# Kernel optimization log

Measured on AMD Instinct MI355X. Metric: run time of the kernel, lower is better.

Reference implementation:

```python
import jax, jax.numpy as jnp
import numpy as np


def setup_inputs() -> dict:
    key = jax.random.key(0)
    kx, ky = jax.random.split(key)
    B, N, M, D = 8, 4096, 4096, 128
    x = jax.random.normal(kx, (B, N, D), dtype=jnp.float32)
    y = jax.random.normal(ky, (B, M, D), dtype=jnp.float32)
    return {"x": x, "y": y}


def reference(x, y):
    # Pairwise L2 distances, equivalent to torch.cdist(x, y) (p=2).
    # ||x_i - y_j||^2 = ||x_i||^2 + ||y_j||^2 - 2 <x_i, y_j>
    x2 = jnp.sum(x * x, axis=-1)[:, :, None]          # [B, N, 1]
    y2 = jnp.sum(y * y, axis=-1)[:, None, :]          # [B, 1, M]
    xy = jnp.einsum("bnd,bmd->bnm", x, y)             # [B, N, M]
    D = jnp.sqrt(jnp.maximum(x2 + y2 - 2.0 * xy, 0.0))  # [B, N, M]
    coverage = D.min(axis=1).mean(axis=-1)            # min over N -> [B, M] -> [B]
    precision = D.min(axis=2).mean(axis=-1)           # min over M -> [B, N] -> [B]
    return (coverage + precision).mean()              # scalar Chamfer loss
```

## Files before the change

kernel.cpp:

```cpp
#include <hip/hip_runtime.h>
#include <cstdint>


#define B_   8
#define N_   4096
#define M_   4096
#define D_   128
#define TPB  8
#define ROWS_PB 256
#define XG   (N_ / ROWS_PB)
#define CHUNKS (M_ / (TPB * 64))

typedef __bf16 bf16x8 __attribute__((ext_vector_type(8)));
typedef float  f32x4  __attribute__((ext_vector_type(4)));
typedef unsigned int u32;

static __device__ __forceinline__ unsigned short f2bf(float f) {
  unsigned u = __float_as_uint(f);
  u += 0x7FFFu + ((u >> 16) & 1u);
  return (unsigned short)(u >> 16);
}

static __device__ __forceinline__ void gld16(void* lds, const void* g) {
  __builtin_amdgcn_global_load_lds(
      (const __attribute__((address_space(1))) void*)g,
      (__attribute__((address_space(3))) void*)lds, 16, 0, 0);
}

__global__ __launch_bounds__(256) void pass1_prep(
    const float* __restrict__ x, const float* __restrict__ y,
    unsigned short* __restrict__ xb, unsigned short* __restrict__ yb,
    float* __restrict__ x2, float* __restrict__ y2)
{
  const int ROWS = B_ * N_;
  int gw   = (blockIdx.x * 256 + threadIdx.x) >> 6;
  int lane = threadIdx.x & 63;
  int half = lane >> 5, sub = lane & 31;
  int row2 = gw * 2 + half;
  bool isx = row2 < ROWS;
  const float* src; unsigned short* dst; float* nrm; int row;
  if (isx) { src = x; dst = xb; nrm = x2; row = row2; }
  else     { src = y; dst = yb; nrm = y2; row = row2 - ROWS; }
  size_t base = (size_t)row * D_ + sub * 4;
  float4 v = *(const float4*)(src + base);
  float sx = isx ? -2.0f : 1.0f;
  u32 p0 = (u32)f2bf(sx * v.x) | ((u32)f2bf(sx * v.y) << 16);
  u32 p1 = (u32)f2bf(sx * v.z) | ((u32)f2bf(sx * v.w) << 16);
  *(uint2*)(dst + base) = make_uint2(p0, p1);
  float s = v.x * v.x + v.y * v.y + v.z * v.z + v.w * v.w;
  #pragma unroll
  for (int m = 1; m < 32; m <<= 1) s += __shfl_xor(s, m, 64);
  if (sub == 0) nrm[row] = s;
}

__global__ __launch_bounds__(256) void pass2_tile(
    const unsigned short* __restrict__ xb, const unsigned short* __restrict__ yb,
    const float* __restrict__ x2, const float* __restrict__ y2,
    float* __restrict__ rowpart, float* __restrict__ colpart)
{
  __shared__ unsigned short ys[2 * 8192];
  __shared__ float cminW[2][16 * 64];

  const int tid  = threadIdx.x;
  const int wave = tid >> 6;
  const int lane = tid & 63;
  const int quad = lane >> 4;
  const int l15  = lane & 15;

  const int id    = blockIdx.x;
  const int b     = id & 7;
  const int xg    = (id >> 3) & 15;
  const int chunk = id >> 7;
  const int n0    = xg * ROWS_PB;
  const int mc0   = chunk * (TPB * 64);

  int srcoff[4], ldsoff[4];
  #pragma unroll
  for (int i = 0; i < 4; ++i) {
    int p  = (wave * 4 + i) * 1024 + lane * 16;
    int r  = p >> 8;
    int pc = (p >> 4) & 15;
    int c  = pc ^ (r & 15);
    srcoff[i] = r * D_ + c * 8;
    ldsoff[i] = (wave * 4 + i) * 1024;
  }

  {
    const unsigned short* src = yb + ((size_t)b * M_ + mc0) * D_;
    #pragma unroll
    for (int i = 0; i < 4; ++i) gld16((char*)ys + ldsoff[i], src + srcoff[i]);
  }

  bf16x8 afrag[4][4];
  const size_t xrow0 = (size_t)b * N_ + n0 + wave * 64;
  #pragma unroll
  for (int kb = 0; kb < 4; ++kb)
    #pragma unroll
    for (int rt = 0; rt < 4; ++rt)
      afrag[kb][rt] = *(const bf16x8*)(xb + (xrow0 + rt * 16 + l15) * D_ + kb * 32 + quad * 8);

  f32x4 xvv[4];
  #pragma unroll
  for (int rt = 0; rt < 4; ++rt)
    #pragma unroll
    for (int r = 0; r < 4; ++r)
      xvv[rt][r] = x2[(size_t)b * N_ + n0 + wave * 64 + rt * 16 + quad * 4 + r];

  const float FINF = __uint_as_float(0x7F800000u);
  float rmin2[4][4];
  #pragma unroll
  for (int rt = 0; rt < 4; ++rt)
    #pragma unroll
    for (int r = 0; r < 4; ++r) rmin2[rt][r] = FINF;

  #pragma unroll 1
  for (int t = 0; t < TPB; ++t) {
    const int m0 = mc0 + t * 64;
    const int d  = (t & 1) * 16384;
    __syncthreads();

    float y2r[4];
    #pragma unroll
    for (int ct = 0; ct < 4; ++ct)
      y2r[ct] = y2[(size_t)b * M_ + m0 + ct * 16 + l15];

    if (t + 1 < TPB) {
      const unsigned short* src = yb + ((size_t)b * M_ + m0 + 64) * D_;
      char* dst = (char*)ys + (16384 - d);
      #pragma unroll
      for (int i = 0; i < 4; ++i) gld16(dst + ldsoff[i], src + srcoff[i]);
    }

    if (t > 0 && tid < 64) {
      const float* cb = cminW[(t - 1) & 1];
      float v = cb[tid];
      #pragma unroll
      for (int w = 1; w < 16; ++w) v = fminf(v, cb[w * 64 + tid]);
      colpart[(size_t)xg * (B_ * M_) + (size_t)b * M_ + (m0 - 64) + tid] = v;
    }

    #pragma unroll
    for (int ct = 0; ct < 4; ++ct) {
      f32x4 a[4];
      #pragma unroll
      for (int rt = 0; rt < 4; ++rt) a[rt] = xvv[rt];
      #pragma unroll
      for (int kb = 0; kb < 4; ++kb) {
        const int row = ct * 16 + l15;
        const int pcB = (kb * 4 + quad) ^ l15;
        bf16x8 bfr = *(const bf16x8*)((const char*)ys + d + row * 256 + pcB * 16);
        #pragma unroll
        for (int rt = 0; rt < 4; ++rt)
          a[rt] = __builtin_amdgcn_mfma_f32_16x16x32_bf16(afrag[kb][rt], bfr, a[rt], 0, 0, 0);
      }
      float yv = y2r[ct];
      float cm = FINF;
      #pragma unroll
      for (int rt = 0; rt < 4; ++rt) {
        #pragma unroll
        for (int r = 0; r < 4; ++r) {
          float s = a[rt][r] + yv;
          rmin2[rt][r] = fminf(rmin2[rt][r], s);
          cm = fminf(cm, s);
        }
      }
      cminW[t & 1][(wave * 4 + quad) * 64 + ct * 16 + l15] = cm;
    }
  }

  __syncthreads();
  if (tid < 64) {
    const float* cb = cminW[(TPB - 1) & 1];
    float v = cb[tid];
    #pragma unroll
    for (int w = 1; w < 16; ++w) v = fminf(v, cb[w * 64 + tid]);
    colpart[(size_t)xg * (B_ * M_) + (size_t)b * M_ + (mc0 + (TPB - 1) * 64) + tid] = v;
  }

  #pragma unroll
  for (int rt = 0; rt < 4; ++rt) {
    #pragma unroll
    for (int r = 0; r < 4; ++r) {
      float v = rmin2[rt][r];
      v = fminf(v, __shfl_xor(v, 1, 64));
      v = fminf(v, __shfl_xor(v, 2, 64));
      v = fminf(v, __shfl_xor(v, 4, 64));
      v = fminf(v, __shfl_xor(v, 8, 64));
      if (l15 == 0)
        rowpart[(size_t)chunk * (B_ * N_) + (size_t)b * N_ + n0 + wave * 64 + rt * 16 + quad * 4 + r] = v;
    }
  }
}

__global__ __launch_bounds__(256) void pass3_final(
    const float* __restrict__ rowpart, const float* __restrict__ colpart,
    float* __restrict__ out)
{
  const int BN = B_ * N_;
  float s1 = 0.0f, s2 = 0.0f;
  for (int i = blockIdx.x * 256 + threadIdx.x; i < BN; i += 64 * 256) {
    float r = rowpart[i];
    #pragma unroll
    for (int c = 1; c < CHUNKS; ++c) r = fminf(r, rowpart[c * BN + i]);
    s1 += sqrtf(fmaxf(r, 0.0f));
    float m = colpart[i];
    #pragma unroll
    for (int g = 1; g < XG; ++g) m = fminf(m, colpart[g * BN + i]);
    s2 += sqrtf(fmaxf(m, 0.0f));
  }
  float s = s1 + s2;
  #pragma unroll
  for (int m = 1; m < 64; m <<= 1) s += __shfl_xor(s, m, 64);
  __shared__ float r1[4];
  int wave = threadIdx.x >> 6, lane = threadIdx.x & 63;
  if (lane == 0) r1[wave] = s;
  __syncthreads();
  if (threadIdx.x == 0)
    atomicAdd(out, (r1[0] + r1[1] + r1[2] + r1[3]) / (float)(B_ * N_));
}

extern "C" void kernel_launch(void* const* d_in, const int* in_sizes, int n_in,
                              void* d_out, int out_size, void* d_ws, size_t ws_size,
                              hipStream_t stream)
{
  const float* x = (const float*)d_in[0];
  const float* y = (const float*)d_in[1];
  char* ws = (char*)d_ws;

  unsigned short* xb = (unsigned short*)(ws);
  unsigned short* yb = (unsigned short*)(ws + (8u << 20));
  float* x2      = (float*)(ws + (16u << 20));
  float* y2      = (float*)(ws + (16u << 20) + (1u << 17));
  float* rowpart = (float*)(ws + (16u << 20) + (2u << 17));
  float* colpart = (float*)(ws + (16u << 20) + (10u << 17));
  float* outf = (float*)d_out;

  hipMemsetAsync(outf, 0, sizeof(float), stream);

  pass1_prep<<<(B_ * N_) / 4, 256, 0, stream>>>(x, y, xb, yb, x2, y2);

  pass2_tile<<<B_ * XG * CHUNKS, 256, 0, stream>>>(xb, yb, x2, y2, rowpart, colpart);

  pass3_final<<<64, 256, 0, stream>>>(rowpart, colpart, outf);
}
```

Measured before the change: 121.2 us.

## Load Y fragments directly from global and reduce column mins with LDS atomics

Removes the double-buffered LDS staging of Y tiles and the per-iteration block barrier. Each wave now reads its bf16 B fragments and y-norms straight from global memory, relying on cache reuse across waves. Column minima are first reduced across quads with shuffles, then merged into a chunk-wide LDS array with atomicMin on the float bit pattern, and written out once at the end. This gives up LDS-level reuse and coalesced staging in exchange for less synchronisation. Comparing floats as unsigned is only order-correct for non-negative values, so slightly negative distances from bf16 rounding may be mis-ordered.

```diff
diff --git a/kernel.cpp b/kernel.cpp
--- a/kernel.cpp
+++ b/kernel.cpp
@@ -19,12 +19,6 @@
   unsigned u = __float_as_uint(f);
   u += 0x7FFFu + ((u >> 16) & 1u);
   return (unsigned short)(u >> 16);
-}
-
-static __device__ __forceinline__ void gld16(void* lds, const void* g) {
-  __builtin_amdgcn_global_load_lds(
-      (const __attribute__((address_space(1))) void*)g,
-      (__attribute__((address_space(3))) void*)lds, 16, 0, 0);
 }
 
 __global__ __launch_bounds__(256) void pass1_prep(
@@ -58,8 +52,7 @@
     const float* __restrict__ x2, const float* __restrict__ y2,
     float* __restrict__ rowpart, float* __restrict__ colpart)
 {
-  __shared__ unsigned short ys[2 * 8192];
-  __shared__ float cminW[2][16 * 64];
+  __shared__ u32 cminS[TPB * 64];
 
   const int tid  = threadIdx.x;
   const int wave = tid >> 6;
@@ -74,22 +67,8 @@
   const int n0    = xg * ROWS_PB;
   const int mc0   = chunk * (TPB * 64);
 
-  int srcoff[4], ldsoff[4];
-  #pragma unroll
-  for (int i = 0; i < 4; ++i) {
-    int p  = (wave * 4 + i) * 1024 + lane * 16;
-    int r  = p >> 8;
-    int pc = (p >> 4) & 15;
-    int c  = pc ^ (r & 15);
-    srcoff[i] = r * D_ + c * 8;
-    ldsoff[i] = (wave * 4 + i) * 1024;
-  }
-
-  {
-    const unsigned short* src = yb + ((size_t)b * M_ + mc0) * D_;
-    #pragma unroll
-    for (int i = 0; i < 4; ++i) gld16((char*)ys + ldsoff[i], src + srcoff[i]);
-  }
+  cminS[tid]       = 0x7F800000u;
+  cminS[tid + 256] = 0x7F800000u;
 
   bf16x8 afrag[4][4];
   const size_t xrow0 = (size_t)b * N_ + n0 + wave * 64;
@@ -113,47 +92,34 @@
     #pragma unroll
     for (int r = 0; r < 4; ++r) rmin2[rt][r] = FINF;
 
+  __syncthreads();
+
+  const unsigned short* ybch = yb + ((size_t)b * M_ + mc0) * D_;
+  const float*          y2ch = y2 + (size_t)b * M_ + mc0;
+
   #pragma unroll 1
   for (int t = 0; t < TPB; ++t) {
-    const int m0 = mc0 + t * 64;
-    const int d  = (t & 1) * 16384;
-    __syncthreads();
-
-    float y2r[4];
-    #pragma unroll
-    for (int ct = 0; ct < 4; ++ct)
-      y2r[ct] = y2[(size_t)b * M_ + m0 + ct * 16 + l15];
-
-    if (t + 1 < TPB) {
-      const unsigned short* src = yb + ((size_t)b * M_ + m0 + 64) * D_;
-      char* dst = (char*)ys + (16384 - d);
-      #pragma unroll
-      for (int i = 0; i < 4; ++i) gld16(dst + ldsoff[i], src + srcoff[i]);
-    }
-
-    if (t > 0 && tid < 64) {
-      const float* cb = cminW[(t - 1) & 1];
-      float v = cb[tid];
-      #pragma unroll
-      for (int w = 1; w < 16; ++w) v = fminf(v, cb[w * 64 + tid]);
-      colpart[(size_t)xg * (B_ * M_) + (size_t)b * M_ + (m0 - 64) + tid] = v;
-    }
+    const int c0 = t * 64;
 
     #pragma unroll
     for (int ct = 0; ct < 4; ++ct) {
+      const int col = c0 + ct * 16 + l15;
+      float yv = y2ch[col];
+      bf16x8 bfr0 = *(const bf16x8*)(ybch + (size_t)col * D_ + 0 * 32 + quad * 8);
+      bf16x8 bfr1 = *(const bf16x8*)(ybch + (size_t)col * D_ + 1 * 32 + quad * 8);
+      bf16x8 bfr2 = *(const bf16x8*)(ybch + (size_t)col * D_ + 2 * 32 + quad * 8);
+      bf16x8 bfr3 = *(const bf16x8*)(ybch + (size_t)col * D_ + 3 * 32 + quad * 8);
+
       f32x4 a[4];
       #pragma unroll
       for (int rt = 0; rt < 4; ++rt) a[rt] = xvv[rt];
       #pragma unroll
-      for (int kb = 0; kb < 4; ++kb) {
-        const int row = ct * 16 + l15;
-        const int pcB = (kb * 4 + quad) ^ l15;
-        bf16x8 bfr = *(const bf16x8*)((const char*)ys + d + row * 256 + pcB * 16);
-        #pragma unroll
-        for (int rt = 0; rt < 4; ++rt)
-          a[rt] = __builtin_amdgcn_mfma_f32_16x16x32_bf16(afrag[kb][rt], bfr, a[rt], 0, 0, 0);
+      for (int rt = 0; rt < 4; ++rt) {
+        a[rt] = __builtin_amdgcn_mfma_f32_16x16x32_bf16(afrag[0][rt], bfr0, a[rt], 0, 0, 0);
+        a[rt] = __builtin_amdgcn_mfma_f32_16x16x32_bf16(afrag[1][rt], bfr1, a[rt], 0, 0, 0);
+        a[rt] = __builtin_amdgcn_mfma_f32_16x16x32_bf16(afrag[2][rt], bfr2, a[rt], 0, 0, 0);
+        a[rt] = __builtin_amdgcn_mfma_f32_16x16x32_bf16(afrag[3][rt], bfr3, a[rt], 0, 0, 0);
       }
-      float yv = y2r[ct];
       float cm = FINF;
       #pragma unroll
       for (int rt = 0; rt < 4; ++rt) {
@@ -164,17 +130,19 @@
           cm = fminf(cm, s);
         }
       }
-      cminW[t & 1][(wave * 4 + quad) * 64 + ct * 16 + l15] = cm;
+      cm = fminf(cm, __shfl_xor(cm, 16, 64));
+      cm = fminf(cm, __shfl_xor(cm, 32, 64));
+      if (lane < 16) atomicMin(&cminS[c0 + ct * 16 + lane], __float_as_uint(cm));
     }
   }
 
   __syncthreads();
-  if (tid < 64) {
-    const float* cb = cminW[(TPB - 1) & 1];
-    float v = cb[tid];
-    #pragma unroll
-    for (int w = 1; w < 16; ++w) v = fminf(v, cb[w * 64 + tid]);
-    colpart[(size_t)xg * (B_ * M_) + (size_t)b * M_ + (mc0 + (TPB - 1) * 64) + tid] = v;
+  {
+    float v0 = __uint_as_float(cminS[tid]);
+    float v1 = __uint_as_float(cminS[tid + 256]);
+    size_t cbase = (size_t)xg * (B_ * M_) + (size_t)b * M_ + mc0;
+    colpart[cbase + tid]       = v0;
+    colpart[cbase + tid + 256] = v1;
   }
 
   #pragma unroll
```

Result: slower. 157.6 us (+29.9%).
